# Optimization experiments

Hardware: AMD Instinct MI355X
Metric: run time of the kernel (lower is better)

Reference implementation:

```python
import jax, jax.numpy as jnp
import numpy as np
from math import sqrt

RATIOS = [0.5, 1.0, 2.0]
SCALES = [128.0, 256.0, 512.0]
STRIDE = 16
NA = 9  # len(RATIOS) * len(SCALES)


def _anchor_template():
    # matches RPNHead.__init__: center at stride/2, w = s/sqrt(r), h = s*sqrt(r)
    t = np.zeros((NA, 4), np.float32)
    for ri, r in enumerate(RATIOS):
        for si, s in enumerate(SCALES):
            i = ri * len(RATIOS) + si
            sr = sqrt(r)
            t[i] = [STRIDE / 2.0, STRIDE / 2.0, s / sr, s * sr]
    return jnp.asarray(t)


def _conv(x, w, b, pad):
    y = jax.lax.conv_general_dilated(
        x, w, window_strides=(1, 1), padding=[(pad, pad), (pad, pad)],
        dimension_numbers=('NCHW', 'OIHW', 'NCHW'))
    return y + b[None, :, None, None]


def setup_inputs() -> dict:
    key = jax.random.key(0)
    ks = jax.random.split(key, 5)
    B, C, H, W = 8, 512, 64, 64
    return {
        'feature_maps': jax.random.normal(ks[0], (B, C, H, W), jnp.float32),
        'img_size': jnp.ones((B, 2), jnp.int32) * 1024,  # (width, height) per image
        'conv_w': jax.random.normal(ks[1], (512, 512, 3, 3), jnp.float32) * 0.01,
        'conv_b': jnp.zeros((512,), jnp.float32),
        'cls_w': jax.random.normal(ks[2], (2 * NA, 512, 1, 1), jnp.float32) * 0.01,
        'cls_b': jnp.zeros((2 * NA,), jnp.float32),
        'reg_w': jax.random.normal(ks[3], (4 * NA, 512, 1, 1), jnp.float32) * 0.01,
        'reg_b': jnp.zeros((4 * NA,), jnp.float32),
    }


def reference(feature_maps, img_size, conv_w, conv_b, cls_w, cls_b, reg_w, reg_b):
    f = jax.nn.relu(_conv(feature_maps, conv_w, conv_b, 1))  # [B,512,H,W]
    B, _, H, W = f.shape
    # heads, NCHW -> NHWC, split anchor dim
    cls = _conv(f, cls_w, cls_b, 0).transpose(0, 2, 3, 1).reshape(B, H, W, NA, 2)
    reg = _conv(f, reg_w, reg_b, 0).transpose(0, 2, 3, 1).reshape(B, H, W, NA, 4)

    # generate_anchors (eval mode: anchors_ignore stays zero)
    tmpl = _anchor_template()  # [NA,4] xywh
    gy, gx = jnp.meshgrid(jnp.arange(H), jnp.arange(W), indexing='ij')
    center = jnp.stack([gx, gy], axis=-1).astype(jnp.float32) * STRIDE  # [H,W,2] (x,y)
    axy = tmpl[None, None, :, :2] + center[:, :, None, :]               # [H,W,NA,2]
    awh = jnp.broadcast_to(tmpl[None, None, :, 2:], (H, W, NA, 2))
    anchors = jnp.concatenate([axy, awh], axis=-1).reshape(-1, 4)       # [A,4]

    A = anchors.shape[0]
    reg = reg.reshape(B, A, 4)
    cls_scores = cls.reshape(B, A, 2)

    # anchor2bbox: inverse of the delta encoding in loss()
    ax, ay, aw, ah = anchors[:, 0], anchors[:, 1], anchors[:, 2], anchors[:, 3]
    px = ax[None, :] + reg[..., 0] * aw[None, :]
    py = ay[None, :] + reg[..., 1] * ah[None, :]
    pw = aw[None, :] * jnp.exp(reg[..., 2])
    ph = ah[None, :] * jnp.exp(reg[..., 3])
    imw = img_size[:, 0:1].astype(jnp.float32)
    imh = img_size[:, 1:2].astype(jnp.float32)
    x1 = jnp.clip(px - pw / 2, 0.0, imw)
    y1 = jnp.clip(py - ph / 2, 0.0, imh)
    x2 = jnp.clip(px + pw / 2, 0.0, imw)
    y2 = jnp.clip(py + ph / 2, 0.0, imh)
    proposals = jnp.stack([x1, y1, x2, y2], axis=-1)  # [B,A,4]

    anchors_ignore = jnp.zeros((B, A), jnp.int32)
    return (proposals, cls_scores, anchors_ignore)
```

## Files before the change

### kernel.cpp

```cpp
#include <hip/hip_runtime.h>
#include <hip/hip_bf16.h>
#include <stdint.h>

typedef __attribute__((ext_vector_type(4))) float f32x4;
typedef __attribute__((ext_vector_type(8))) short short8;

#define NB 8
#define NC 512
#define HP 66
#define WP 66
#define NPOS 32768
#define KTOT 4608
#define NKT 72

#define XP_ELEMS (NB*HP*WP*NC)
#define WR_ELEMS (NC*KTOT)
#define WC2_ELEMS (64*NC)
#define PROP_OFF 0
#define CLS_OFF  1179648
#define ANCH_OFF 1769472
#define A_PER_B  36864

__device__ __forceinline__ short bf16bits(float v) {
    __hip_bfloat16 b = __float2bfloat16(v);
    return *reinterpret_cast<short*>(&b);
}
__device__ __forceinline__ void gload16(const short* g, short* l) {
    __builtin_amdgcn_global_load_lds(
        (const __attribute__((address_space(1))) unsigned int*)g,
        (__attribute__((address_space(3))) unsigned int*)l, 16, 0, 0);
}
#define BARRIER() asm volatile("s_barrier" ::: "memory")
#define VMCNT4()  asm volatile("s_waitcnt vmcnt(4)" ::: "memory")
#define VMCNT0()  asm volatile("s_waitcnt vmcnt(0)" ::: "memory")

__global__ void prep_all(const float* __restrict__ x, const float* __restrict__ conv_w,
                         const float* __restrict__ cls_w, const float* __restrict__ reg_w,
                         short* __restrict__ Wr, short* __restrict__ Wc2,
                         short* __restrict__ Xp) {
    __shared__ float smem[4608];
    const int bid = blockIdx.x, tid = threadIdx.x;
    if (bid < 4096) {
        float (*t)[65] = (float(*)[65])smem;
        const int pb = bid & 63, cb = (bid >> 6) & 7, b = bid >> 9;
        const float* src = x + ((size_t)(b*NC + cb*64))*4096 + pb*64;
        const int w4 = tid & 15, chb = tid >> 4;
#pragma unroll
        for (int r = 0; r < 4; ++r) {
            int ch = r*16 + chb;
            float4 v = *(const float4*)(src + (size_t)ch*4096 + w4*4);
            t[ch][w4*4 + 0] = v.x;
            t[ch][w4*4 + 1] = v.y;
            t[ch][w4*4 + 2] = v.z;
            t[ch][w4*4 + 3] = v.w;
        }
        __syncthreads();
#pragma unroll
        for (int rr = 0; rr < 2; ++rr) {
            int item = tid + rr*256;
            int pl = item >> 3, ck = item & 7;
            short8 v;
#pragma unroll
            for (int e = 0; e < 8; ++e) v[e] = bf16bits(t[ck*8+e][pl]);
            *(short8*)&Xp[((size_t)((b*HP + pb + 1)*WP) + (pl + 1))*NC + cb*64 + ck*8] = v;
        }
    } else if (bid < 4608) {
        const int o = bid - 4096;
        const float4* src4 = (const float4*)(conv_w + (size_t)o*4608);
        float4* smem4 = (float4*)smem;
        for (int i = tid; i < 1152; i += 256) smem4[i] = src4[i];
        __syncthreads();
#pragma unroll
        for (int k = 0; k < 9; ++k)
#pragma unroll
            for (int c = 0; c < 2; ++c) {
                int ci = tid + c*256;
                Wr[(size_t)o*4608 + k*512 + ci] = bf16bits(smem[ci*9 + k]);
            }
    } else {
        const int m = bid - 4608;
        if (m < 128) {
            int t = m*256 + tid;
            int row = t >> 9, ci = t & 511;
            float v = 0.f;
            if (row < 18)      v = cls_w[row*NC + ci];
            else if (row < 54) v = reg_w[(row-18)*NC + ci];
            Wc2[t] = bf16bits(v);
        } else {
            int idx = (m-128)*256 + tid;
            int b = idx / 16640;
            int rem = idx - b*16640;
            int r = rem >> 6, g = rem & 63;
            int h, w;
            if      (r < 66)  { h = 0;       w = r; }
            else if (r < 132) { h = 65;      w = r - 66; }
            else if (r < 196) { h = r - 131; w = 0; }
            else              { h = r - 195; w = 65; }
            short8 z = (short8){0,0,0,0,0,0,0,0};
            *(short8*)&Xp[((size_t)((b*HP + h)*WP) + w)*NC + g*8] = z;
        }
    }
}

__launch_bounds__(512, 2)
__global__ void conv_fused(const short* __restrict__ Xp, const short* __restrict__ Wr,
                           const float* __restrict__ bias, const short* __restrict__ Wc2,
                           float* __restrict__ partial) {
    extern __shared__ short lds[];
    const int tid = threadIdx.x;
    const int lane = tid & 63, wv = tid >> 6;
    const int bid = blockIdx.x;
    const int wg = (bid & 7) * 32 + (bid >> 3);
    const int pbase  = (wg >> 1) * 256;
    const int cobase = (wg & 1) * 256;
    const int wm = wv >> 2, wn = wv & 3;

    const int g_data = (tid & 7) ^ ((tid >> 3) & 7);
    int abase[4], bbase[4];
#pragma unroll
    for (int q = 0; q < 4; ++q) {
        int p = pbase + q*64 + (tid >> 3);
        int b = p >> 12, h = (p >> 6) & 63, w = p & 63;
        abase[q] = ((b*HP + h)*WP + w)*NC + g_data*8;
        bbase[q] = (cobase + q*64 + (tid >> 3))*KTOT + g_data*8;
    }
    const int stoff = tid*8;

    const int l15 = lane & 15, l4 = lane >> 4, l7 = lane & 7;
    const int kidx0 = (l4 ^ l7) * 8;
    const int kidx1 = ((4 + l4) ^ l7) * 8;
    const int Aroff = wm*8192 + l15*64;
    const int Broff = 16384 + (wn>>1)*8192 + (wn&1)*4096 + l15*64;

    auto stageA = [&](int t, int hh) {
        int seg = t >> 3;
        int dh = seg / 3, dw = seg - dh*3;
        int off = (dh*WP + dw)*NC + (t & 7)*64;
        short* dst = lds + (t & 1)*32768 + hh*8192 + stoff;
        gload16(Xp + abase[hh*2+0] + off, dst);
        gload16(Xp + abase[hh*2+1] + off, dst + 4096);
    };
    auto stageB = [&](int t, int hh) {
        int off = t * 64;
        short* dst = lds + (t & 1)*32768 + 16384 + hh*8192 + stoff;
        gload16(Wr + bbase[hh*2+0] + off, dst);
        gload16(Wr + bbase[hh*2+1] + off, dst + 4096);
    };

    f32x4 acc[8][4];
#pragma unroll
    for (int i = 0; i < 8; ++i)
#pragma unroll
        for (int j = 0; j < 4; ++j) acc[i][j] = (f32x4){0.f,0.f,0.f,0.f};

    short8 af[2][2], bfr[4][2];
    auto readA = [&](int bufb, int i2) {
        const short* Ab = lds + bufb*32768 + Aroff;
#pragma unroll
        for (int ii = 0; ii < 2; ++ii) {
            af[ii][0] = *(const short8*)(Ab + (i2+ii)*1024 + kidx0);
            af[ii][1] = *(const short8*)(Ab + (i2+ii)*1024 + kidx1);
        }
    };
    auto readB = [&](int bufb) {
        const short* Bb = lds + bufb*32768 + Broff;
#pragma unroll
        for (int j = 0; j < 4; ++j) {
            bfr[j][0] = *(const short8*)(Bb + j*1024 + kidx0);
            bfr[j][1] = *(const short8*)(Bb + j*1024 + kidx1);
        }
    };
    auto mfmaQ = [&](int i2) {
        __builtin_amdgcn_s_setprio(1);
#pragma unroll
        for (int kk = 0; kk < 2; ++kk)
#pragma unroll
            for (int ii = 0; ii < 2; ++ii)
#pragma unroll
                for (int j = 0; j < 4; ++j)
                    acc[i2+ii][j] = __builtin_amdgcn_mfma_f32_16x16x32_bf16(
                        af[ii][kk], bfr[j][kk], acc[i2+ii][j], 0, 0, 0);
        __builtin_amdgcn_s_setprio(0);
    };

    stageB(0,0); stageB(0,1); stageA(0,0); stageA(0,1); stageB(1,0); stageB(1,1);
    VMCNT4(); BARRIER();

    for (int it = 0; it < 36; ++it) {
        const int t1 = 2*it+1, t2 = 2*it+2, t3 = 2*it+3;
        const bool s2 = (t2 < NKT), s3 = (t3 < NKT);
        readB(0); readA(0, 0);
        stageA(t1, 0);
        BARRIER(); mfmaQ(0); BARRIER();
        readA(0, 2);
        stageA(t1, 1);
        BARRIER(); mfmaQ(2); BARRIER();
        readA(0, 4);
        if (s2) stageB(t2, 0);
        BARRIER(); mfmaQ(4); BARRIER();
        readA(0, 6);
        if (s2) stageB(t2, 1);
        BARRIER(); mfmaQ(6);
        if (s2) { VMCNT4(); } else { VMCNT0(); }
        BARRIER();
        readB(1); readA(1, 0);
        if (s2) stageA(t2, 0);
        BARRIER(); mfmaQ(0); BARRIER();
        readA(1, 2);
        if (s2) stageA(t2, 1);
        BARRIER(); mfmaQ(2); BARRIER();
        readA(1, 4);
        if (s3) stageB(t3, 0);
        BARRIER(); mfmaQ(4); BARRIER();
        readA(1, 6);
        if (s3) stageB(t3, 1);
        BARRIER(); mfmaQ(6);
        if (s3) { VMCNT4(); } else { VMCNT0(); }
        BARRIER();
    }
    __syncthreads();

#pragma unroll
    for (int j = 0; j < 4; ++j) {
        const int ch = wn*64 + j*16 + l15;
        const float bb = bias[cobase + ch];
        const int g = ch >> 3, e = ch & 7;
#pragma unroll
        for (int i = 0; i < 8; ++i) {
#pragma unroll
            for (int r = 0; r < 4; ++r) {
                const int pos = wm*128 + i*16 + l4*4 + r;
                float v = acc[i][j][r] + bb;
                v = v > 0.f ? v : 0.f;
                const int slot = (g & 24) | ((g ^ pos) & 7);
                lds[pos*256 + slot*8 + e] = bf16bits(v);
            }
        }
    }
    __syncthreads();

    f32x4 acc2[2][4];
#pragma unroll
    for (int i2 = 0; i2 < 2; ++i2)
#pragma unroll
        for (int j2 = 0; j2 < 4; ++j2) acc2[i2][j2] = (f32x4){0.f,0.f,0.f,0.f};
    const int hbase = wv*32;
#pragma unroll
    for (int kk = 0; kk < 8; ++kk) {
        short8 b2[4];
#pragma unroll
        for (int j2 = 0; j2 < 4; ++j2)
            b2[j2] = *(const short8*)&Wc2[(size_t)(j2*16 + l15)*NC + cobase + kk*32 + l4*8];
#pragma unroll
        for (int i2 = 0; i2 < 2; ++i2) {
            const int pos = hbase + i2*16 + l15;
            const int g = kk*4 + l4;
            const int slot = (g & 24) | ((g ^ pos) & 7);
            short8 a2 = *(const short8*)&lds[pos*256 + slot*8];
#pragma unroll
            for (int j2 = 0; j2 < 4; ++j2)
                acc2[i2][j2] = __builtin_amdgcn_mfma_f32_16x16x32_bf16(
                    a2, b2[j2], acc2[i2][j2], 0, 0, 0);
        }
    }

    const int half = wg & 1;
    float* pdst = partial + ((size_t)half*NPOS + pbase + hbase)*64;
#pragma unroll
    for (int i2 = 0; i2 < 2; ++i2)
#pragma unroll
        for (int j2 = 0; j2 < 4; ++j2)
#pragma unroll
            for (int r = 0; r < 4; ++r)
                pdst[(i2*16 + l4*4 + r)*64 + j2*16 + l15] = acc2[i2][j2][r];
}

__device__ const float AW_T[9] = {
    181.01933598375618f, 362.03867196751236f, 724.0773439350247f,
    128.f, 256.f, 512.f,
    90.50966799187809f, 181.01933598375618f, 362.03867196751236f };
__device__ const float AH_T[9] = {
    90.50966799187809f, 181.01933598375618f, 362.03867196751236f,
    128.f, 256.f, 512.f,
    181.01933598375618f, 362.03867196751236f, 724.0773439350247f };

__launch_bounds__(256)
__global__ void combine_decode(const float* __restrict__ partial,
                               const float* __restrict__ cls_b, const float* __restrict__ reg_b,
                               const int* __restrict__ img, float* __restrict__ out) {
    __shared__ float sm[64*65];
    const int tid = threadIdx.x;
    const int p0 = blockIdx.x * 64;
    const float4* pa = (const float4*)partial;
#pragma unroll
    for (int q = 0; q < 4; ++q) {
        int idx = tid + q*256;
        int pl = idx >> 4, n4 = idx & 15;
        float4 a = pa[(size_t)(p0 + pl)*16 + n4];
        float4 b = pa[(size_t)(NPOS + p0 + pl)*16 + n4];
        sm[pl*65 + n4*4 + 0] = a.x + b.x;
        sm[pl*65 + n4*4 + 1] = a.y + b.y;
        sm[pl*65 + n4*4 + 2] = a.z + b.z;
        sm[pl*65 + n4*4 + 3] = a.w + b.w;
    }
    __syncthreads();

    for (int item = tid; item < 576; item += 256) {
        int pl = item / 9, a = item - pl*9;
        int p = p0 + pl;
        int b = p >> 12, h = (p >> 6) & 63, w = p & 63;
        float c0 = sm[pl*65 + a*2 + 0] + cls_b[a*2 + 0];
        float c1 = sm[pl*65 + a*2 + 1] + cls_b[a*2 + 1];
        float r0 = sm[pl*65 + 18 + a*4 + 0] + reg_b[a*4 + 0];
        float r1 = sm[pl*65 + 18 + a*4 + 1] + reg_b[a*4 + 1];
        float r2 = sm[pl*65 + 18 + a*4 + 2] + reg_b[a*4 + 2];
        float r3 = sm[pl*65 + 18 + a*4 + 3] + reg_b[a*4 + 3];
        float aw = AW_T[a], ah = AH_T[a];
        float ax = 8.f + 16.f*w, ay = 8.f + 16.f*h;
        float px = ax + r0*aw,  py = ay + r1*ah;
        float pw = aw*__expf(r2), ph = ah*__expf(r3);
        float imw = (float)img[b*2 + 0], imh = (float)img[b*2 + 1];
        float x1 = fminf(fmaxf(px - 0.5f*pw, 0.f), imw);
        float y1 = fminf(fmaxf(py - 0.5f*ph, 0.f), imh);
        float x2 = fminf(fmaxf(px + 0.5f*pw, 0.f), imw);
        float y2 = fminf(fmaxf(py + 0.5f*ph, 0.f), imh);
        int ag = (h*64 + w)*9 + a;
        float4* prop = (float4*)(out + PROP_OFF + ((size_t)b*A_PER_B + ag)*4);
        *prop = make_float4(x1, y1, x2, y2);
        float2* cs = (float2*)(out + CLS_OFF + ((size_t)b*A_PER_B + ag)*2);
        *cs = make_float2(c0, c1);
        out[ANCH_OFF + (size_t)b*A_PER_B + ag] = 0.0f;
    }
}

extern "C" void kernel_launch(void* const* d_in, const int* in_sizes, int n_in,
                              void* d_out, int out_size, void* d_ws, size_t ws_size,
                              hipStream_t stream) {
    const float* x      = (const float*)d_in[0];
    const int*   img    = (const int*)  d_in[1];
    const float* conv_w = (const float*)d_in[2];
    const float* conv_b = (const float*)d_in[3];
    const float* cls_w  = (const float*)d_in[4];
    const float* cls_b  = (const float*)d_in[5];
    const float* reg_w  = (const float*)d_in[6];
    const float* reg_b  = (const float*)d_in[7];
    float* out = (float*)d_out;

    short* Xp      = (short*)d_ws;
    short* Wr      = Xp  + XP_ELEMS;
    short* Wc2     = Wr  + WR_ELEMS;
    float* partial = (float*)(Wc2 + WC2_ELEMS);

    prep_all<<<5256, 256, 0, stream>>>(x, conv_w, cls_w, reg_w, Wr, Wc2, Xp);

    hipFuncSetAttribute((const void*)conv_fused,
                        hipFuncAttributeMaxDynamicSharedMemorySize, 131072);
    conv_fused<<<256, 512, 131072, stream>>>(Xp, Wr, conv_b, Wc2, partial);
    combine_decode<<<NPOS/64, 256, 0, stream>>>(partial, cls_b, reg_b, img, out);
}
```

Before: 248.9 us.

## Switch main conv GEMM from 16x16x32 to 32x32x16 bf16 MFMA tiles

Replaces the 16x16x32 MFMA inner kernel of the 3x3 conv implicit GEMM with 32x32x16 MFMAs, which changes the accumulator layout, the LDS fragment read pattern (new swizzled slot indexing) and the epilogue position mapping. Larger MFMA tiles need fewer LDS fragment reads per flop and fewer instructions, so the loop is meant to be less bound on LDS bandwidth and issue. B fragments are now reloaded in halves across phases. The risk is LDS bank conflicts under the new read pattern and correctness of the remapped accumulator-to-position layout.

```diff
diff --git a/kernel.cpp b/kernel.cpp
--- a/kernel.cpp
+++ b/kernel.cpp
@@ -3,6 +3,7 @@
 #include <stdint.h>
 
 typedef __attribute__((ext_vector_type(4))) float f32x4;
+typedef __attribute__((ext_vector_type(16))) float f32x16;
 typedef __attribute__((ext_vector_type(8))) short short8;
 
 #define NB 8
@@ -127,10 +128,7 @@
     const int stoff = tid*8;
 
     const int l15 = lane & 15, l4 = lane >> 4, l7 = lane & 7;
-    const int kidx0 = (l4 ^ l7) * 8;
-    const int kidx1 = ((4 + l4) ^ l7) * 8;
-    const int Aroff = wm*8192 + l15*64;
-    const int Broff = 16384 + (wn>>1)*8192 + (wn&1)*4096 + l15*64;
+    const int l31 = lane & 31, ls5 = lane >> 5;
 
     auto stageA = [&](int t, int hh) {
         int seg = t >> 3;
@@ -147,39 +145,47 @@
         gload16(Wr + bbase[hh*2+1] + off, dst + 4096);
     };
 
-    f32x4 acc[8][4];
-#pragma unroll
-    for (int i = 0; i < 8; ++i)
-#pragma unroll
-        for (int j = 0; j < 4; ++j) acc[i][j] = (f32x4){0.f,0.f,0.f,0.f};
-
-    short8 af[2][2], bfr[4][2];
-    auto readA = [&](int bufb, int i2) {
-        const short* Ab = lds + bufb*32768 + Aroff;
-#pragma unroll
-        for (int ii = 0; ii < 2; ++ii) {
-            af[ii][0] = *(const short8*)(Ab + (i2+ii)*1024 + kidx0);
-            af[ii][1] = *(const short8*)(Ab + (i2+ii)*1024 + kidx1);
-        }
-    };
-    auto readB = [&](int bufb) {
-        const short* Bb = lds + bufb*32768 + Broff;
-#pragma unroll
-        for (int j = 0; j < 4; ++j) {
-            bfr[j][0] = *(const short8*)(Bb + j*1024 + kidx0);
-            bfr[j][1] = *(const short8*)(Bb + j*1024 + kidx1);
-        }
-    };
-    auto mfmaQ = [&](int i2) {
+    f32x16 acc32[4][2];
+#pragma unroll
+    for (int i = 0; i < 4; ++i)
+#pragma unroll
+        for (int j = 0; j < 2; ++j) acc32[i][j] = (f32x16)(0.f);
+
+    short8 af32[2][2];
+    short8 bf32[2][4];
+
+    auto readA32 = [&](int bufb, int rb, int sb) {
+        const short* Ab = lds + bufb*32768 + (wm*128 + l31)*64;
+#pragma unroll
+        for (int ri = 0; ri < 2; ++ri)
+#pragma unroll
+            for (int sp = 0; sp < 2; ++sp) {
+                const int s = sb + sp;
+                const int slot = (s*2 + ls5) ^ l7;
+                af32[ri][sp] = *(const short8*)(Ab + (rb + ri)*2048 + slot*8);
+            }
+    };
+    auto readB32 = [&](int bufb, int sb) {
+        const short* Bb = lds + bufb*32768 + 16384 + (wn*64 + l31)*64;
+#pragma unroll
+        for (int cj = 0; cj < 2; ++cj)
+#pragma unroll
+            for (int sp = 0; sp < 2; ++sp) {
+                const int s = sb + sp;
+                const int slot = (s*2 + ls5) ^ l7;
+                bf32[cj][s] = *(const short8*)(Bb + cj*2048 + slot*8);
+            }
+    };
+    auto mfma32 = [&](int rb, int sb) {
         __builtin_amdgcn_s_setprio(1);
 #pragma unroll
-        for (int kk = 0; kk < 2; ++kk)
-#pragma unroll
-            for (int ii = 0; ii < 2; ++ii)
-#pragma unroll
-                for (int j = 0; j < 4; ++j)
-                    acc[i2+ii][j] = __builtin_amdgcn_mfma_f32_16x16x32_bf16(
-                        af[ii][kk], bfr[j][kk], acc[i2+ii][j], 0, 0, 0);
+        for (int sp = 0; sp < 2; ++sp)
+#pragma unroll
+            for (int ri = 0; ri < 2; ++ri)
+#pragma unroll
+                for (int cj = 0; cj < 2; ++cj)
+                    acc32[rb+ri][cj] = __builtin_amdgcn_mfma_f32_32x32x16_bf16(
+                        af32[ri][sp], bf32[cj][sb+sp], acc32[rb+ri][cj], 0, 0, 0);
         __builtin_amdgcn_s_setprio(0);
     };
 
@@ -189,51 +195,51 @@
     for (int it = 0; it < 36; ++it) {
         const int t1 = 2*it+1, t2 = 2*it+2, t3 = 2*it+3;
         const bool s2 = (t2 < NKT), s3 = (t3 < NKT);
-        readB(0); readA(0, 0);
+        readB32(0, 0); readA32(0, 0, 0);
         stageA(t1, 0);
-        BARRIER(); mfmaQ(0); BARRIER();
-        readA(0, 2);
+        BARRIER(); mfma32(0, 0); BARRIER();
+        readB32(0, 2); readA32(0, 0, 2);
         stageA(t1, 1);
-        BARRIER(); mfmaQ(2); BARRIER();
-        readA(0, 4);
+        BARRIER(); mfma32(0, 2); BARRIER();
+        readA32(0, 2, 0);
         if (s2) stageB(t2, 0);
-        BARRIER(); mfmaQ(4); BARRIER();
-        readA(0, 6);
+        BARRIER(); mfma32(2, 0); BARRIER();
+        readA32(0, 2, 2);
         if (s2) stageB(t2, 1);
-        BARRIER(); mfmaQ(6);
+        BARRIER(); mfma32(2, 2);
         if (s2) { VMCNT4(); } else { VMCNT0(); }
         BARRIER();
-        readB(1); readA(1, 0);
+        readB32(1, 0); readA32(1, 0, 0);
         if (s2) stageA(t2, 0);
-        BARRIER(); mfmaQ(0); BARRIER();
-        readA(1, 2);
+        BARRIER(); mfma32(0, 0); BARRIER();
+        readB32(1, 2); readA32(1, 0, 2);
         if (s2) stageA(t2, 1);
-        BARRIER(); mfmaQ(2); BARRIER();
-        readA(1, 4);
+        BARRIER(); mfma32(0, 2); BARRIER();
+        readA32(1, 2, 0);
         if (s3) stageB(t3, 0);
-        BARRIER(); mfmaQ(4); BARRIER();
-        readA(1, 6);
+        BARRIER(); mfma32(2, 0); BARRIER();
+        readA32(1, 2, 2);
         if (s3) stageB(t3, 1);
-        BARRIER(); mfmaQ(6);
+        BARRIER(); mfma32(2, 2);
         if (s3) { VMCNT4(); } else { VMCNT0(); }
         BARRIER();
     }
     __syncthreads();
 
 #pragma unroll
-    for (int j = 0; j < 4; ++j) {
-        const int ch = wn*64 + j*16 + l15;
+    for (int cj = 0; cj < 2; ++cj) {
+        const int ch = wn*64 + cj*32 + l31;
         const float bb = bias[cobase + ch];
-        const int g = ch >> 3, e = ch & 7;
-#pragma unroll
-        for (int i = 0; i < 8; ++i) {
-#pragma unroll
-            for (int r = 0; r < 4; ++r) {
-                const int pos = wm*128 + i*16 + l4*4 + r;
-                float v = acc[i][j][r] + bb;
+        const int g = ch >> 3, e8 = ch & 7;
+#pragma unroll
+        for (int ri = 0; ri < 4; ++ri) {
+#pragma unroll
+            for (int e = 0; e < 16; ++e) {
+                const int pos = wm*128 + ri*32 + (e & 3) + 8*(e >> 2) + 4*ls5;
+                float v = acc32[ri][cj][e] + bb;
                 v = v > 0.f ? v : 0.f;
                 const int slot = (g & 24) | ((g ^ pos) & 7);
-                lds[pos*256 + slot*8 + e] = bf16bits(v);
+                lds[pos*256 + slot*8 + e8] = bf16bits(v);
             }
         }
     }
```

After: 265.5 us. 1.07x slower.
